# Kernel optimization log

Measured on AMD Instinct MI355X. Metric: run time of the kernel, lower is better.

Reference implementation:

```python
import jax, jax.numpy as jnp
import numpy as np

NUE, NAP, E = 512, 1024, 524288
D, OC, HID, PH = 4, 64, 32, 4  # raw feat dim, out_channels, out//2, power hid


def _lin(key, fi, fo):
    k1, k2 = jax.random.split(key)
    s = 1.0 / np.sqrt(fi)
    W = jax.random.uniform(k1, (fi, fo), minval=-s, maxval=s, dtype=jnp.float32)
    b = jax.random.uniform(k2, (fo,), minval=-s, maxval=s, dtype=jnp.float32)
    return W, b


_LAYER_SPECS = [
    ("c1_msg", D + D, HID), ("c1_upd", HID + D, OC - D), ("c1_ew", 3 * D, OC - D),
    ("c2_msg", OC + D, HID), ("c2_upd", HID + D, OC - D), ("c2_ew", D + OC + D, OC - D),
    ("c3u_msg", 2 * OC, HID), ("c3u_upd", HID + OC, OC - D), ("c3u_ew", 3 * OC, OC - D),
    ("c3d_msg", 2 * OC, HID), ("c3d_upd", HID + OC, OC - D), ("c3d_ew", 3 * OC, OC - D),
    ("pe1", OC, PH), ("pe2", PH, 1),
]


def setup_inputs() -> dict:
    key = jax.random.key(0)
    ks = jax.random.split(key, 24)
    inp = {}
    inp["x_ue"] = jax.random.normal(ks[0], (NUE, D), dtype=jnp.float32)
    inp["x_ap"] = jax.random.normal(ks[1], (NAP, D), dtype=jnp.float32)
    inp["ea_up"] = jax.random.normal(ks[2], (E, D), dtype=jnp.float32)
    inp["ea_down"] = jax.random.normal(ks[3], (E, D), dtype=jnp.float32)
    inp["ei_up_src"] = jax.random.randint(ks[4], (E,), 0, NUE, dtype=jnp.int32)
    inp["ei_up_dst"] = jax.random.randint(ks[5], (E,), 0, NAP, dtype=jnp.int32)
    inp["ei_down_src"] = jax.random.randint(ks[6], (E,), 0, NAP, dtype=jnp.int32)
    inp["ei_down_dst"] = jax.random.randint(ks[7], (E,), 0, NUE, dtype=jnp.int32)
    for i, (n, fi, fo) in enumerate(_LAYER_SPECS):
        W, b = _lin(ks[8 + i], fi, fo)
        inp[n + "_W"] = W
        inp[n + "_b"] = b
    inp["pe_ln_g"] = jnp.ones((PH,), dtype=jnp.float32)
    inp["pe_ln_b"] = jnp.zeros((PH,), dtype=jnp.float32)
    return inp


def _lrelu(x):
    return jnp.where(x >= 0, x, 0.1 * x)


def _mlp1(x, W, b):  # one MLP block: Linear -> LeakyReLU(0.1) (dropout = eval identity)
    return _lrelu(x @ W + b)


def _conv_step(x_src, x_dst, ea, src_idx, dst_idx, n_dst,
               msg_W, msg_b, upd_W, upd_b, ew_W, ew_b, residual):
    xj = x_src[src_idx]                                   # [E, d_src] gather
    m = _mlp1(jnp.concatenate([xj, ea], axis=1), msg_W, msg_b)  # [E, HID]
    agg = jax.ops.segment_sum(m, dst_idx, num_segments=n_dst)   # scatter-add -> [n_dst, HID]
    tmp = _mlp1(jnp.concatenate([x_dst, agg], axis=1), upd_W, upd_b)  # [n_dst, OC-D]
    if residual:
        tmp = tmp + x_dst[:, D:]
    new_x_dst = jnp.concatenate([x_dst[:, :D], tmp], axis=1)     # [n_dst, OC]
    xi = x_dst[dst_idx]                                   # old x_dst per torch code
    e = _mlp1(jnp.concatenate([xj, ea, xi], axis=1), ew_W, ew_b)  # [E, OC-D]
    new_ea = jnp.concatenate([ea[:, :D], e], axis=1)             # [E, OC]
    return new_x_dst, new_ea


def _layernorm(x, g, b, eps=1e-5):
    mu = jnp.mean(x, axis=-1, keepdims=True)
    var = jnp.mean(jnp.square(x - mu), axis=-1, keepdims=True)
    return (x - mu) * jax.lax.rsqrt(var + eps) * g + b


def reference(x_ue, x_ap, ea_up, ea_down,
              ei_up_src, ei_up_dst, ei_down_src, ei_down_dst,
              c1_msg_W, c1_msg_b, c1_upd_W, c1_upd_b, c1_ew_W, c1_ew_b,
              c2_msg_W, c2_msg_b, c2_upd_W, c2_upd_b, c2_ew_W, c2_ew_b,
              c3u_msg_W, c3u_msg_b, c3u_upd_W, c3u_upd_b, c3u_ew_W, c3u_ew_b,
              c3d_msg_W, c3d_msg_b, c3d_upd_W, c3d_upd_b, c3d_ew_W, c3d_ew_b,
              pe1_W, pe1_b, pe2_W, pe2_b, pe_ln_g, pe_ln_b):
    # conv1: UE --up--> AP
    x_ap, ea_up = _conv_step(x_ue, x_ap, ea_up, ei_up_src, ei_up_dst, NAP,
                             c1_msg_W, c1_msg_b, c1_upd_W, c1_upd_b, c1_ew_W, c1_ew_b, False)
    # conv2: AP --down--> UE
    x_ue, ea_down = _conv_step(x_ap, x_ue, ea_down, ei_down_src, ei_down_dst, NUE,
                               c2_msg_W, c2_msg_b, c2_upd_W, c2_upd_b, c2_ew_W, c2_ew_b, False)
    # conv3 handles both edge types (residual since src_dim == out_channels)
    x_ap, ea_up = _conv_step(x_ue, x_ap, ea_up, ei_up_src, ei_up_dst, NAP,
                             c3u_msg_W, c3u_msg_b, c3u_upd_W, c3u_upd_b, c3u_ew_W, c3u_ew_b, True)
    x_ue, ea_down = _conv_step(x_ap, x_ue, ea_down, ei_down_src, ei_down_dst, NUE,
                               c3d_msg_W, c3d_msg_b, c3d_upd_W, c3d_upd_b, c3d_ew_W, c3d_ew_b, True)
    # power head on down edges: Lin -> LayerNorm -> LeakyReLU -> Lin
    h = _lrelu(_layernorm(ea_down @ pe1_W + pe1_b, pe_ln_g, pe_ln_b))
    power = h @ pe2_W + pe2_b                                   # [E, 1]
    ea_down = jnp.concatenate([ea_down[:, :D], power], axis=1)  # [E, D+1]
    return (x_ue, x_ap, ea_up, ea_down)
```

## Files before the change

### kernel.cpp

```cpp
#include <hip/hip_runtime.h>

typedef __attribute__((ext_vector_type(8))) short bf16x8;
typedef __attribute__((ext_vector_type(4))) float f32x4;

static constexpr int EN   = 524288;
static constexpr int NUE_ = 512;
static constexpr int NAP_ = 1024;
static constexpr int HID_ = 32;
static constexpr int OD_  = 60;
static constexpr int OC_  = 64;
static constexpr int NB_  = 256;
static constexpr int CH_  = EN / NB_;

__device__ __forceinline__ unsigned short f2bf(float x) {
  unsigned int u = __float_as_uint(x);
  return (unsigned short)((u + 0x7fffu + ((u >> 16) & 1u)) >> 16);
}
__device__ __forceinline__ float bf2f(unsigned int u) {
  return __uint_as_float(u << 16);
}

__global__ __launch_bounds__(256)
void prep_all(const float* __restrict__ c3u_ew, const float* __restrict__ c3u_msg,
              const float* __restrict__ c3d_ew, const float* __restrict__ c3d_msg,
              unsigned short* __restrict__ we3u, unsigned short* __restrict__ wm3u,
              unsigned short* __restrict__ we3d, unsigned short* __restrict__ wm3d)
{
  const int blk = blockIdx.x, t = threadIdx.x;
  const float* W; unsigned short* out; int NREAL, NPAD, i;
  if (blk < 16)      { W = c3u_ew;  out = we3u; NREAL = 60; NPAD = 64; i = blk * 256 + t; }
  else if (blk < 24) { W = c3u_msg; out = wm3u; NREAL = 32; NPAD = 32; i = (blk - 16) * 256 + t; }
  else if (blk < 40) { W = c3d_ew;  out = we3d; NREAL = 60; NPAD = 64; i = (blk - 24) * 256 + t; }
  else               { W = c3d_msg; out = wm3d; NREAL = 32; NPAD = 32; i = (blk - 40) * 256 + t; }
  if (i >= NPAD * 64) return;
  int n = i >> 6, k = i & 63;
  float v = (n < NREAL) ? W[(size_t)(64 + k) * NREAL + n] : 0.f;
  out[i] = f2bf(v);
}

__global__ __launch_bounds__(256)
void lhist2(const int* __restrict__ up_dst, const int* __restrict__ dn_dst,
            int* __restrict__ bh_up, int* __restrict__ bh_dn,
            unsigned short* __restrict__ lr_up, unsigned short* __restrict__ lr_dn)
{
  __shared__ int h[NAP_];
  const int t = threadIdx.x;
  const bool up = blockIdx.x < NB_;
  const int b = up ? blockIdx.x : blockIdx.x - NB_;
  const int NBINS = up ? NAP_ : NUE_;
  const int* dst = up ? up_dst : dn_dst;
  int* bh = up ? bh_up : bh_dn;
  unsigned short* lrank = up ? lr_up : lr_dn;
  for (int i = t; i < NBINS; i += 256) h[i] = 0;
  __syncthreads();
  const int base = b * CH_;
  #pragma unroll 1
  for (int i = t; i < CH_; i += 256)
    lrank[base + i] = (unsigned short)atomicAdd(&h[dst[base + i]], 1);
  __syncthreads();
  for (int i = t; i < NBINS; i += 256)
    bh[(size_t)i * NB_ + b] = h[i];
}

__global__ __launch_bounds__(64)
void bscanA2(int* __restrict__ bh_up, int* __restrict__ bh_dn,
             int* __restrict__ bs_up, int* __restrict__ bs_dn)
{
  const bool up = blockIdx.x < NAP_;
  const int bin = up ? blockIdx.x : blockIdx.x - NAP_;
  int* bh = up ? bh_up : bh_dn;
  int* binsum = up ? bs_up : bs_dn;
  const int l = threadIdx.x;
  int4 v = *reinterpret_cast<int4*>(&bh[(size_t)bin * NB_ + l * 4]);
  const int s0 = v.x, s1 = s0 + v.y, s2 = s1 + v.z, s3 = s2 + v.w;
  int inc = s3;
  #pragma unroll
  for (int d2 = 1; d2 < 64; d2 <<= 1) {
    int n = __shfl_up(inc, d2, 64);
    if (l >= d2) inc += n;
  }
  const int exc = inc - s3;
  int4 o; o.x = exc; o.y = exc + s0; o.z = exc + s1; o.w = exc + s2;
  *reinterpret_cast<int4*>(&bh[(size_t)bin * NB_ + l * 4]) = o;
  if (l == 63) binsum[bin] = inc;
}

__global__ __launch_bounds__(256)
void bscanB2(const int* __restrict__ bs_up, int* __restrict__ off_up,
             const int* __restrict__ bs_dn, int* __restrict__ off_dn)
{
  const bool up = blockIdx.x == 0;
  const int NBINS = up ? NAP_ : NUE_;
  const int K = NBINS / 256;
  const int* binsum = up ? bs_up : bs_dn;
  int* off = up ? off_up : off_dn;
  __shared__ int wtot[4];
  const int t = threadIdx.x, lane = t & 63, wid = t >> 6;
  int loc[4]; int s = 0;
  for (int k = 0; k < K; ++k) { loc[k] = binsum[t * K + k]; s += loc[k]; }
  int inc = s;
  #pragma unroll
  for (int d2 = 1; d2 < 64; d2 <<= 1) {
    int n = __shfl_up(inc, d2, 64);
    if (lane >= d2) inc += n;
  }
  if (lane == 63) wtot[wid] = inc;
  __syncthreads();
  int woff = 0;
  #pragma unroll
  for (int ww = 0; ww < 4; ++ww) if (ww < wid) woff += wtot[ww];
  int a = woff + inc - s;
  for (int k = 0; k < K; ++k) { off[t * K + k] = a; a += loc[k]; }
  if (t == 255) off[NBINS] = a;
}

__global__ __launch_bounds__(256)
void rankc2(const int* __restrict__ up_dst, const int* __restrict__ up_src,
            const int* __restrict__ dn_dst, const int* __restrict__ dn_src,
            const unsigned short* __restrict__ lr_up, const unsigned short* __restrict__ lr_dn,
            const int* __restrict__ bh_up, const int* __restrict__ bh_dn,
            const int* __restrict__ off_up, const int* __restrict__ off_dn,
            int* __restrict__ rank_dn,
            int* __restrict__ perm_up, int* __restrict__ srcP_up, int* __restrict__ dstP_up,
            int* __restrict__ perm_dn, int* __restrict__ srcP_dn, int* __restrict__ dstP_dn)
{
  const int gid = blockIdx.x * 256 + threadIdx.x;
  const bool up = gid < EN;
  const int e = up ? gid : gid - EN;
  const int* dst = up ? up_dst : dn_dst;
  const int* src = up ? up_src : dn_src;
  const unsigned short* lrank = up ? lr_up : lr_dn;
  const int* bh = up ? bh_up : bh_dn;
  const int* off = up ? off_up : off_dn;
  const int blk = e / CH_;
  const int d = dst[e];
  const int rk = off[d] + bh[(size_t)d * NB_ + blk] + (int)lrank[e];
  if (up) {
    perm_up[rk] = e; srcP_up[rk] = src[e]; dstP_up[rk] = d;
  } else {
    rank_dn[e] = rk;
    perm_dn[rk] = e; srcP_dn[rk] = src[e]; dstP_dn[rk] = d;
  }
}

__global__ __launch_bounds__(256)
void tabs0(const float* __restrict__ x_ue, const float* __restrict__ x_ap,
           const float* __restrict__ c1_ew, const float* __restrict__ c1_msg,
           const float* __restrict__ c1_ew_b, const float* __restrict__ c1_msg_b,
           const float* __restrict__ c2_ew, const float* __restrict__ c2_ew_b,
           float* __restrict__ Y1j, float* __restrict__ Y1i,
           float* __restrict__ Y1m, float* __restrict__ Y2i)
{
  const int tid = blockIdx.x * 256 + threadIdx.x;
  if (tid < NUE_) {
    const float4 x = *reinterpret_cast<const float4*>(x_ue + (size_t)tid * 4);
    const float xv[4] = {x.x, x.y, x.z, x.w};
    for (int o = 0; o < OD_; ++o) {
      float a = 0.f, b = c2_ew_b[o];
      #pragma unroll
      for (int k = 0; k < 4; ++k) {
        a = fmaf(xv[k], c1_ew[k * OD_ + o], a);
        b = fmaf(xv[k], c2_ew[(68 + k) * OD_ + o], b);
      }
      Y1j[(size_t)tid * OD_ + o] = a;
      Y2i[(size_t)tid * OD_ + o] = b;
    }
    for (int o = 0; o < HID_; ++o) {
      float m = c1_msg_b[o];
      #pragma unroll
      for (int k = 0; k < 4; ++k) m = fmaf(xv[k], c1_msg[k * HID_ + o], m);
      Y1m[(size_t)tid * HID_ + o] = m;
    }
  } else if (tid < NUE_ + NAP_) {
    const int r = tid - NUE_;
    const float4 x = *reinterpret_cast<const float4*>(x_ap + (size_t)r * 4);
    const float xv[4] = {x.x, x.y, x.z, x.w};
    for (int o = 0; o < OD_; ++o) {
      float a = c1_ew_b[o];
      #pragma unroll
      for (int k = 0; k < 4; ++k) a = fmaf(xv[k], c1_ew[(8 + k) * OD_ + o], a);
      Y1i[(size_t)r * OD_ + o] = a;
    }
  }
}

__global__ __launch_bounds__(256)
void edge12(const float* __restrict__ ea_in,
            const int* __restrict__ perm, const int* __restrict__ srcP,
            const int* __restrict__ dstP,
            const float* __restrict__ Yje, const float* __restrict__ Yie,
            const float* __restrict__ Ym,
            const float* __restrict__ We,
            const float* __restrict__ Wm,
            unsigned int* __restrict__ msg32,
            unsigned short* __restrict__ outB)
{
  __shared__ unsigned short Eb[64 * 72];
  const int t = threadIdx.x;
  const int sBase = blockIdx.x * 64;
  const int r = t >> 2, j = t & 3;
  const int slot = sBase + r;
  const int e = perm[slot];
  const int s = srcP[slot], d = dstP[slot];
  const float4 ea = *reinterpret_cast<const float4*>(ea_in + (size_t)e * 4);
  const float eav[4] = {ea.x, ea.y, ea.z, ea.w};

  const int c0 = j * 15;
  float acc[15];
  #pragma unroll
  for (int c = 0; c < 15; ++c)
    acc[c] = Yje[(size_t)s * OD_ + c0 + c] + Yie[(size_t)d * OD_ + c0 + c];
  #pragma unroll
  for (int k = 0; k < 4; ++k)
    #pragma unroll
    for (int c = 0; c < 15; ++c)
      acc[c] = fmaf(eav[k], We[k * OD_ + c0 + c], acc[c]);
  #pragma unroll
  for (int c = 0; c < 15; ++c) {
    float v = acc[c] >= 0.f ? acc[c] : 0.1f * acc[c];
    Eb[r * 72 + 4 + c0 + c] = f2bf(v);
  }
  if (j == 0) {
    Eb[r * 72 + 0] = f2bf(ea.x); Eb[r * 72 + 1] = f2bf(ea.y);
    Eb[r * 72 + 2] = f2bf(ea.z); Eb[r * 72 + 3] = f2bf(ea.w);
  }
  const int m0 = j * 8;
  float m[8];
  #pragma unroll
  for (int c = 0; c < 8; ++c) m[c] = Ym[(size_t)s * HID_ + m0 + c];
  #pragma unroll
  for (int k = 0; k < 4; ++k)
    #pragma unroll
    for (int c = 0; c < 8; ++c)
      m[c] = fmaf(eav[k], Wm[k * HID_ + m0 + c], m[c]);
  #pragma unroll
  for (int c = 0; c < 8; ++c) m[c] = m[c] >= 0.f ? m[c] : 0.1f * m[c];
  uint4 mv;
  mv.x = ((unsigned)f2bf(m[1]) << 16) | f2bf(m[0]);
  mv.y = ((unsigned)f2bf(m[3]) << 16) | f2bf(m[2]);
  mv.z = ((unsigned)f2bf(m[5]) << 16) | f2bf(m[4]);
  mv.w = ((unsigned)f2bf(m[7]) << 16) | f2bf(m[6]);
  *reinterpret_cast<uint4*>(msg32 + (size_t)slot * 16 + j * 4) = mv;
  __syncthreads();

  #pragma unroll
  for (int i = 0; i < 2; ++i) {
    int idx = t + i * 256;
    int row = idx >> 3, ch = idx & 7;
    *reinterpret_cast<uint4*>(outB + (size_t)(sBase + row) * OC_ + ch * 8) =
        *reinterpret_cast<const uint4*>(&Eb[row * 72 + ch * 8]);
  }
}

template<bool FUSE>
__global__ __launch_bounds__(256)
void edge3(const unsigned short* __restrict__ eaB,
           const float* __restrict__ ea0_src,
           const int* __restrict__ perm,
           const int* __restrict__ srcP, const int* __restrict__ dstP,
           const unsigned short* __restrict__ Wet, const unsigned short* __restrict__ Wmt,
           const float* __restrict__ Yje, const float* __restrict__ Yie,
           const float* __restrict__ Ym,
           unsigned int* __restrict__ msg32,
           float* __restrict__ ea_out,
           float* __restrict__ pT,
           const float* __restrict__ pe1_W)
{
  const int t = threadIdx.x, l = t & 63, w = t >> 6;
  const int lr = l & 15, lkb = l >> 4;
  const int sW = blockIdx.x * 256 + w * 64;

  bf16x8 be[4][2], bm[2][2];
  #pragma unroll
  for (int nt = 0; nt < 4; ++nt)
    #pragma unroll
    for (int kk = 0; kk < 2; ++kk)
      be[nt][kk] = *reinterpret_cast<const bf16x8*>(Wet + (nt * 16 + lr) * 64 + kk * 32 + lkb * 8);
  #pragma unroll
  for (int nt = 0; nt < 2; ++nt)
    #pragma unroll
    for (int kk = 0; kk < 2; ++kk)
      bm[nt][kk] = *reinterpret_cast<const bf16x8*>(Wmt + (nt * 16 + lr) * 64 + kk * 32 + lkb * 8);

  #pragma unroll 1
  for (int tile = 0; tile < 4; ++tile) {
    const int s0t = sW + tile * 16;
    const unsigned short* ar = eaB + (size_t)(s0t + lr) * OC_ + lkb * 8;
    bf16x8 a[2];
    a[0] = *reinterpret_cast<const bf16x8*>(ar);
    a[1] = *reinterpret_cast<const bf16x8*>(ar + 32);

    f32x4 accE[4] = {f32x4{0,0,0,0}, f32x4{0,0,0,0}, f32x4{0,0,0,0}, f32x4{0,0,0,0}};
    f32x4 accM[2] = {f32x4{0,0,0,0}, f32x4{0,0,0,0}};
    #pragma unroll
    for (int kk = 0; kk < 2; ++kk) {
      #pragma unroll
      for (int nt = 0; nt < 4; ++nt)
        accE[nt] = __builtin_amdgcn_mfma_f32_16x16x32_bf16(a[kk], be[nt][kk], accE[nt], 0, 0, 0);
      #pragma unroll
      for (int nt = 0; nt < 2; ++nt)
        accM[nt] = __builtin_amdgcn_mfma_f32_16x16x32_bf16(a[kk], bm[nt][kk], accM[nt], 0, 0, 0);
    }
    #pragma unroll
    for (int r = 0; r < 4; ++r) {
      const int sl = s0t + lkb * 4 + r;
      const int s = srcP[sl], d = dstP[sl];
      float v0 = accM[0][r] + Ym[(size_t)s * HID_ + lr];
      float v1 = accM[1][r] + Ym[(size_t)s * HID_ + 16 + lr];
      v0 = v0 >= 0.f ? v0 : 0.1f * v0;
      v1 = v1 >= 0.f ? v1 : 0.1f * v1;
      const int q0 = (2 * lr) & 15, q1 = (2 * lr + 1) & 15;
      float t00 = __shfl(v0, q0, 16), t10 = __shfl(v1, q0, 16);
      float t01 = __shfl(v0, q1, 16), t11 = __shfl(v1, q1, 16);
      float lo = (lr < 8) ? t00 : t10;
      float hi = (lr < 8) ? t01 : t11;
      msg32[(size_t)sl * 16 + lr] = ((unsigned)f2bf(hi) << 16) | f2bf(lo);

      float val[4];
      #pragma unroll
      for (int nt = 0; nt < 4; ++nt) {
        int col = nt * 16 + lr;
        float v = (col < OD_)
            ? accE[nt][r] + Yje[(size_t)s * OD_ + col] + Yie[(size_t)d * OD_ + col]
            : 0.f;
        val[nt] = v >= 0.f ? v : 0.1f * v;
      }
      if constexpr (!FUSE) {
        const int e = perm[sl];
        #pragma unroll
        for (int nt = 0; nt < 4; ++nt) {
          int col = nt * 16 + lr;
          if (col < OD_) ea_out[(size_t)e * OC_ + 4 + col] = val[nt];
        }
        if (lr == 0) {
          float4 ea0 = *reinterpret_cast<const float4*>(ea0_src + (size_t)e * 4);
          *reinterpret_cast<float4*>(ea_out + (size_t)e * OC_) = ea0;
        }
      } else {
        float p4[4] = {0.f, 0.f, 0.f, 0.f};
        #pragma unroll
        for (int nt = 0; nt < 4; ++nt) {
          int col = nt * 16 + lr;
          if (col < OD_) {
            #pragma unroll
            for (int jj = 0; jj < 4; ++jj)
              p4[jj] = fmaf(val[nt], pe1_W[(4 + col) * 4 + jj], p4[jj]);
          }
        }
        #pragma unroll
        for (int mk = 1; mk < 16; mk <<= 1) {
          #pragma unroll
          for (int jj = 0; jj < 4; ++jj)
            p4[jj] += __shfl_xor(p4[jj], mk, 64);
        }
        if (lr == 0)
          *reinterpret_cast<float4*>(pT + (size_t)sl * 4) =
              make_float4(p4[0], p4[1], p4[2], p4[3]);
      }
    }
  }
}

template<int LX, bool RES>
__device__ __forceinline__
void nodeup_body(int d, int t,
                 const float* __restrict__ x_in,
                 const unsigned int* __restrict__ msg32,
                 const int* __restrict__ off,
                 const float* __restrict__ W, const float* __restrict__ b,
                 float* __restrict__ x_out,
                 const float* WtA, float* YA,
                 const float* WtB, const float* bB, float* YB,
                 const float* WtC, const float* bC, float* YC)
{
  __shared__ float Pb[16][32];
  __shared__ float Ag[32];
  __shared__ float Xr[LX];
  __shared__ float Xn[OC_];
  const int beg = off[d], end = off[d + 1];
  const int c = t & 15, g = t >> 4;
  float px = 0.f, py = 0.f;
  for (int i = beg + g; i < end; i += 16) {
    unsigned u = msg32[(size_t)i * 16 + c];
    px += bf2f(u & 0xffffu);
    py += bf2f(u >> 16);
  }
  Pb[g][2 * c] = px; Pb[g][2 * c + 1] = py;
  if (t < LX) Xr[t] = x_in[(size_t)d * LX + t];
  __syncthreads();
  if (t < 32) {
    float s = 0.f;
    #pragma unroll
    for (int g2 = 0; g2 < 16; ++g2) s += Pb[g2][t];
    Ag[t] = s;
  }
  __syncthreads();
  if (t < OD_) {
    float acc = b[t];
    #pragma unroll 4
    for (int k = 0; k < LX; ++k) acc = fmaf(Xr[k], W[k * OD_ + t], acc);
    #pragma unroll 4
    for (int k = 0; k < HID_; ++k) acc = fmaf(Ag[k], W[(LX + k) * OD_ + t], acc);
    acc = acc >= 0.f ? acc : 0.1f * acc;
    if constexpr (RES) acc += Xr[4 + t];
    x_out[(size_t)d * OC_ + 4 + t] = acc;
    Xn[4 + t] = acc;
  } else if (t < OC_) {
    x_out[(size_t)d * OC_ + (t - OD_)] = Xr[t - OD_];
    Xn[t - OD_] = Xr[t - OD_];
  }
  if (WtA == nullptr) return;
  __syncthreads();
  if (t < OD_) {
    float a = 0.f;
    #pragma unroll 4
    for (int k = 0; k < OC_; ++k) a = fmaf(Xn[k], WtA[k * OD_ + t], a);
    YA[(size_t)d * OD_ + t] = a;
  } else if (t >= 64 && t < 96) {
    const int cc = t - 64;
    float a = bB[cc];
    #pragma unroll 4
    for (int k = 0; k < OC_; ++k) a = fmaf(Xn[k], WtB[k * HID_ + cc], a);
    YB[(size_t)d * HID_ + cc] = a;
  } else if (WtC != nullptr && t >= 128 && t < 188) {
    const int cc = t - 128;
    float a = bC[cc];
    #pragma unroll 4
    for (int k = 0; k < OC_; ++k) a = fmaf(Xn[k], WtC[k * OD_ + cc], a);
    YC[(size_t)d * OD_ + cc] = a;
  }
}

template<int LX, bool RES>
__global__ __launch_bounds__(256)
void nodeupT(const float* __restrict__ x_in, const unsigned int* __restrict__ msg32,
             const int* __restrict__ off,
             const float* __restrict__ W, const float* __restrict__ b,
             float* __restrict__ x_out,
             const float* WtA, float* YA,
             const float* WtB, const float* bB, float* YB,
             const float* WtC, const float* bC, float* YC)
{
  nodeup_body<LX, RES>(blockIdx.x, threadIdx.x, x_in, msg32, off, W, b, x_out,
                       WtA, YA, WtB, bB, YB, WtC, bC, YC);
}

__global__ __launch_bounds__(256)
void nodeup_pow(const float* __restrict__ x_in, const unsigned int* __restrict__ msg32,
                const int* __restrict__ off,
                const float* __restrict__ W, const float* __restrict__ b,
                float* __restrict__ x_out,
                const float* __restrict__ ea0_src, const int* __restrict__ rank,
                const float* __restrict__ pT,
                const float* __restrict__ pe1_W, const float* __restrict__ pe1_b,
                const float* __restrict__ pe2_W, const float* __restrict__ pe2_b,
                const float* __restrict__ ln_g, const float* __restrict__ ln_b,
                float* __restrict__ outp)
{
  if (blockIdx.x < NUE_) {
    nodeup_body<OC_, true>(blockIdx.x, threadIdx.x, x_in, msg32, off, W, b, x_out,
                           nullptr, nullptr, nullptr, nullptr, nullptr,
                           nullptr, nullptr, nullptr);
    return;
  }
  const int e = (blockIdx.x - NUE_) * 256 + threadIdx.x;
  const int rk = rank[e];
  const float4 p4 = *reinterpret_cast<const float4*>(pT + (size_t)rk * 4);
  const float4 ea0 = *reinterpret_cast<const float4*>(ea0_src + (size_t)e * 4);
  const float pv[4] = {p4.x, p4.y, p4.z, p4.w};
  float v4[4];
  #pragma unroll
  for (int jj = 0; jj < 4; ++jj)
    v4[jj] = pv[jj] + pe1_b[jj]
           + ea0.x * pe1_W[0 * 4 + jj] + ea0.y * pe1_W[1 * 4 + jj]
           + ea0.z * pe1_W[2 * 4 + jj] + ea0.w * pe1_W[3 * 4 + jj];
  const float mu = 0.25f * (v4[0] + v4[1] + v4[2] + v4[3]);
  float var = 0.f;
  #pragma unroll
  for (int jj = 0; jj < 4; ++jj) { float dd = v4[jj] - mu; var = fmaf(dd, dd, var); }
  var *= 0.25f;
  const float rstd = rsqrtf(var + 1e-5f);
  float p = pe2_b[0];
  #pragma unroll
  for (int jj = 0; jj < 4; ++jj) {
    float h = (v4[jj] - mu) * rstd * ln_g[jj] + ln_b[jj];
    h = h >= 0.f ? h : 0.1f * h;
    p = fmaf(h, pe2_W[jj], p);
  }
  float* orow = outp + (size_t)e * 5;
  orow[0] = ea0.x; orow[1] = ea0.y; orow[2] = ea0.z; orow[3] = ea0.w;
  orow[4] = p;
}

extern "C" void kernel_launch(void* const* d_in, const int* in_sizes, int n_in,
                              void* d_out, int out_size, void* d_ws, size_t ws_size,
                              hipStream_t stream)
{
  const float* x_ue    = (const float*)d_in[0];
  const float* x_ap    = (const float*)d_in[1];
  const float* ea_up   = (const float*)d_in[2];
  const float* ea_down = (const float*)d_in[3];
  const int* up_src = (const int*)d_in[4];
  const int* up_dst = (const int*)d_in[5];
  const int* dn_src = (const int*)d_in[6];
  const int* dn_dst = (const int*)d_in[7];
  const float* c1_msg_W = (const float*)d_in[8];  const float* c1_msg_b = (const float*)d_in[9];
  const float* c1_upd_W = (const float*)d_in[10]; const float* c1_upd_b = (const float*)d_in[11];
  const float* c1_ew_W  = (const float*)d_in[12]; const float* c1_ew_b  = (const float*)d_in[13];
  const float* c2_msg_W = (const float*)d_in[14]; const float* c2_msg_b = (const float*)d_in[15];
  const float* c2_upd_W = (const float*)d_in[16]; const float* c2_upd_b = (const float*)d_in[17];
  const float* c2_ew_W  = (const float*)d_in[18]; const float* c2_ew_b  = (const float*)d_in[19];
  const float* c3u_msg_W= (const float*)d_in[20]; const float* c3u_msg_b= (const float*)d_in[21];
  const float* c3u_upd_W= (const float*)d_in[22]; const float* c3u_upd_b= (const float*)d_in[23];
  const float* c3u_ew_W = (const float*)d_in[24]; const float* c3u_ew_b = (const float*)d_in[25];
  const float* c3d_msg_W= (const float*)d_in[26]; const float* c3d_msg_b= (const float*)d_in[27];
  const float* c3d_upd_W= (const float*)d_in[28]; const float* c3d_upd_b= (const float*)d_in[29];
  const float* c3d_ew_W = (const float*)d_in[30]; const float* c3d_ew_b = (const float*)d_in[31];
  const float* pe1_W = (const float*)d_in[32]; const float* pe1_b = (const float*)d_in[33];
  const float* pe2_W = (const float*)d_in[34]; const float* pe2_b = (const float*)d_in[35];
  const float* ln_g  = (const float*)d_in[36]; const float* ln_b  = (const float*)d_in[37];

  float* out    = (float*)d_out;
  float* x_ue_o = out;
  float* x_ap_o = out + (size_t)NUE_ * OC_;
  float* ea_up_o = x_ap_o + (size_t)NAP_ * OC_;
  float* ea_dn_o = ea_up_o + (size_t)EN * OC_;

  int* ip = (int*)d_ws;
  int* rank_dn = ip; ip += EN;
  int* perm_up = ip; ip += EN;
  int* src_upP = ip; ip += EN;
  int* dst_upP = ip; ip += EN;
  int* perm_dn = ip; ip += EN;
  int* src_dnP = ip; ip += EN;
  int* dst_dnP = ip; ip += EN;
  int* bh_up   = ip; ip += NAP_ * NB_;
  int* bh_dn   = ip; ip += NUE_ * NB_;
  int* off_up  = ip; ip += NAP_ + 1;
  int* off_dn  = ip; ip += NUE_ + 1;
  int* bs_up   = ip; ip += NAP_;
  int* bs_dn   = ip; ip += NUE_;
  unsigned short* lr_up = (unsigned short*)ip; ip += EN / 2;
  unsigned short* lr_dn = (unsigned short*)ip; ip += EN / 2;
  float* p = (float*)ip;
  float* Y1j = p;  p += NUE_ * OD_;  float* Y1i = p; p += NAP_ * OD_;  float* Y1m = p; p += NUE_ * HID_;
  float* Y2j = p;  p += NAP_ * OD_;  float* Y2i = p; p += NUE_ * OD_;  float* Y2m = p; p += NAP_ * HID_;
  float* Y3uj = p; p += NUE_ * OD_;  float* Y3ui = p; p += NAP_ * OD_; float* Y3um = p; p += NUE_ * HID_;
  float* Y3dj = p; p += NAP_ * OD_;  float* Y3di = p; p += NUE_ * OD_; float* Y3dm = p; p += NAP_ * HID_;
  float* pT = p;   p += (size_t)EN * 4;
  unsigned short* us = (unsigned short*)p;
  unsigned short* ea_up_bf = us;  us += (size_t)EN * OC_;
  unsigned short* ea_dn_bf = us;  us += (size_t)EN * OC_;
  unsigned short* we3u = us; us += 64 * 64;
  unsigned short* wm3u = us; us += 32 * 64;
  unsigned short* we3d = us; us += 64 * 64;
  unsigned short* wm3d = us; us += 32 * 64;
  unsigned int* msg32 = (unsigned int*)(((size_t)us + 15) & ~(size_t)15);

  const dim3 blk(256);
  const dim3 eg12(EN / 64);
  const dim3 ege(EN / 256);

  lhist2<<<dim3(2 * NB_), blk, 0, stream>>>(up_dst, dn_dst, bh_up, bh_dn, lr_up, lr_dn);
  bscanA2<<<dim3(NAP_ + NUE_), dim3(64), 0, stream>>>(bh_up, bh_dn, bs_up, bs_dn);
  bscanB2<<<dim3(2), blk, 0, stream>>>(bs_up, off_up, bs_dn, off_dn);
  rankc2<<<dim3(2 * EN / 256), blk, 0, stream>>>(
      up_dst, up_src, dn_dst, dn_src, lr_up, lr_dn, bh_up, bh_dn, off_up, off_dn,
      rank_dn, perm_up, src_upP, dst_upP, perm_dn, src_dnP, dst_dnP);

  prep_all<<<dim3(48), blk, 0, stream>>>(c3u_ew_W, c3u_msg_W, c3d_ew_W, c3d_msg_W,
                                         we3u, wm3u, we3d, wm3d);
  tabs0<<<dim3(8), blk, 0, stream>>>(x_ue, x_ap, c1_ew_W, c1_msg_W, c1_ew_b, c1_msg_b,
                                     c2_ew_W, c2_ew_b, Y1j, Y1i, Y1m, Y2i);

  edge12<<<eg12, blk, 0, stream>>>(
      ea_up, perm_up, src_upP, dst_upP, Y1j, Y1i, Y1m,
      c1_ew_W + 4 * OD_, c1_msg_W + 4 * HID_, msg32, ea_up_bf);
  nodeupT<4, false><<<dim3(NAP_), blk, 0, stream>>>(
      x_ap, msg32, off_up, c1_upd_W, c1_upd_b, x_ap_o,
      c2_ew_W, Y2j, c2_msg_W, c2_msg_b, Y2m,
      c3u_ew_W + 128 * OD_, c3u_ew_b, Y3ui);

  edge12<<<eg12, blk, 0, stream>>>(
      ea_down, perm_dn, src_dnP, dst_dnP, Y2j, Y2i, Y2m,
      c2_ew_W + 64 * OD_, c2_msg_W + 64 * HID_, msg32, ea_dn_bf);
  nodeupT<4, false><<<dim3(NUE_), blk, 0, stream>>>(
      x_ue, msg32, off_dn, c2_upd_W, c2_upd_b, x_ue_o,
      c3u_ew_W, Y3uj, c3u_msg_W, c3u_msg_b, Y3um,
      c3d_ew_W + 128 * OD_, c3d_ew_b, Y3di);

  edge3<false><<<ege, blk, 0, stream>>>(
      ea_up_bf, ea_up, perm_up, src_upP, dst_upP, we3u, wm3u,
      Y3uj, Y3ui, Y3um, msg32, ea_up_o, nullptr, nullptr);
  nodeupT<64, true><<<dim3(NAP_), blk, 0, stream>>>(
      x_ap_o, msg32, off_up, c3u_upd_W, c3u_upd_b, x_ap_o,
      c3d_ew_W, Y3dj, c3d_msg_W, c3d_msg_b, Y3dm,
      nullptr, nullptr, nullptr);

  edge3<true><<<ege, blk, 0, stream>>>(
      ea_dn_bf, nullptr, nullptr, src_dnP, dst_dnP, we3d, wm3d,
      Y3dj, Y3di, Y3dm, msg32, nullptr, pT, pe1_W);
  nodeup_pow<<<dim3(NUE_ + EN / 256), blk, 0, stream>>>(
      x_ue_o, msg32, off_dn, c3d_upd_W, c3d_upd_b, x_ue_o,
      ea_down, rank_dn, pT, pe1_W, pe1_b, pe2_W, pe2_b, ln_g, ln_b, ea_dn_o);
}
```

Before: 471.5 us.

## Fuse conv1/conv2 edge pass with per-destination aggregation and node update

Replaces the edge12 plus nodeupT pair for conv1 and conv2 with a single e12n kernel that runs one block per destination node. Each block walks that node's sorted edge segment, writes the edge features, and accumulates messages in registers, which removes the msg32 round trip and one launch per conv. The small prep and table kernels are folded into extra blocks of the histogram kernel, and edge3 now prefetches its A tiles and src/dst indices ahead of the MFMA loop. The trade-off is parallelism: conv1 gets only 1024 blocks and conv2 only 512, each with a serial loop over about 512 or 1024 edges, so load balance and occupancy may suffer compared with the edge-parallel grid.

```diff
diff --git a/kernel.cpp b/kernel.cpp
--- a/kernel.cpp
+++ b/kernel.cpp
@@ -21,30 +21,69 @@
 }
 
 __global__ __launch_bounds__(256)
-void prep_all(const float* __restrict__ c3u_ew, const float* __restrict__ c3u_msg,
-              const float* __restrict__ c3d_ew, const float* __restrict__ c3d_msg,
-              unsigned short* __restrict__ we3u, unsigned short* __restrict__ wm3u,
-              unsigned short* __restrict__ we3d, unsigned short* __restrict__ wm3d)
-{
-  const int blk = blockIdx.x, t = threadIdx.x;
-  const float* W; unsigned short* out; int NREAL, NPAD, i;
-  if (blk < 16)      { W = c3u_ew;  out = we3u; NREAL = 60; NPAD = 64; i = blk * 256 + t; }
-  else if (blk < 24) { W = c3u_msg; out = wm3u; NREAL = 32; NPAD = 32; i = (blk - 16) * 256 + t; }
-  else if (blk < 40) { W = c3d_ew;  out = we3d; NREAL = 60; NPAD = 64; i = (blk - 24) * 256 + t; }
-  else               { W = c3d_msg; out = wm3d; NREAL = 32; NPAD = 32; i = (blk - 40) * 256 + t; }
-  if (i >= NPAD * 64) return;
-  int n = i >> 6, k = i & 63;
-  float v = (n < NREAL) ? W[(size_t)(64 + k) * NREAL + n] : 0.f;
-  out[i] = f2bf(v);
-}
-
-__global__ __launch_bounds__(256)
-void lhist2(const int* __restrict__ up_dst, const int* __restrict__ dn_dst,
-            int* __restrict__ bh_up, int* __restrict__ bh_dn,
-            unsigned short* __restrict__ lr_up, unsigned short* __restrict__ lr_dn)
+void lhist2x(const int* __restrict__ up_dst, const int* __restrict__ dn_dst,
+             int* __restrict__ bh_up, int* __restrict__ bh_dn,
+             unsigned short* __restrict__ lr_up, unsigned short* __restrict__ lr_dn,
+             const float* __restrict__ c3u_ew, const float* __restrict__ c3u_msg,
+             const float* __restrict__ c3d_ew, const float* __restrict__ c3d_msg,
+             unsigned short* __restrict__ we3u, unsigned short* __restrict__ wm3u,
+             unsigned short* __restrict__ we3d, unsigned short* __restrict__ wm3d,
+             const float* __restrict__ x_ue, const float* __restrict__ x_ap,
+             const float* __restrict__ c1_ew, const float* __restrict__ c1_msg,
+             const float* __restrict__ c1_ew_b, const float* __restrict__ c1_msg_b,
+             const float* __restrict__ c2_ew, const float* __restrict__ c2_ew_b,
+             float* __restrict__ Y1j, float* __restrict__ Y1i,
+             float* __restrict__ Y1m, float* __restrict__ Y2i)
 {
   __shared__ int h[NAP_];
   const int t = threadIdx.x;
+  if (blockIdx.x >= 2 * NB_) {
+    const int xb = blockIdx.x - 2 * NB_;
+    if (xb < 48) {
+      const float* W; unsigned short* out; int NREAL, NPAD, i;
+      if (xb < 16)      { W = c3u_ew;  out = we3u; NREAL = 60; NPAD = 64; i = xb * 256 + t; }
+      else if (xb < 24) { W = c3u_msg; out = wm3u; NREAL = 32; NPAD = 32; i = (xb - 16) * 256 + t; }
+      else if (xb < 40) { W = c3d_ew;  out = we3d; NREAL = 60; NPAD = 64; i = (xb - 24) * 256 + t; }
+      else              { W = c3d_msg; out = wm3d; NREAL = 32; NPAD = 32; i = (xb - 40) * 256 + t; }
+      if (i >= NPAD * 64) return;
+      int n = i >> 6, k = i & 63;
+      float v = (n < NREAL) ? W[(size_t)(64 + k) * NREAL + n] : 0.f;
+      out[i] = f2bf(v);
+    } else {
+      const int tid = (xb - 48) * 256 + t;
+      if (tid < NUE_) {
+        const float4 x = *reinterpret_cast<const float4*>(x_ue + (size_t)tid * 4);
+        const float xv[4] = {x.x, x.y, x.z, x.w};
+        for (int o = 0; o < OD_; ++o) {
+          float a = 0.f, bb = c2_ew_b[o];
+          #pragma unroll
+          for (int k = 0; k < 4; ++k) {
+            a = fmaf(xv[k], c1_ew[k * OD_ + o], a);
+            bb = fmaf(xv[k], c2_ew[(68 + k) * OD_ + o], bb);
+          }
+          Y1j[(size_t)tid * OD_ + o] = a;
+          Y2i[(size_t)tid * OD_ + o] = bb;
+        }
+        for (int o = 0; o < HID_; ++o) {
+          float m = c1_msg_b[o];
+          #pragma unroll
+          for (int k = 0; k < 4; ++k) m = fmaf(xv[k], c1_msg[k * HID_ + o], m);
+          Y1m[(size_t)tid * HID_ + o] = m;
+        }
+      } else if (tid < NUE_ + NAP_) {
+        const int r = tid - NUE_;
+        const float4 x = *reinterpret_cast<const float4*>(x_ap + (size_t)r * 4);
+        const float xv[4] = {x.x, x.y, x.z, x.w};
+        for (int o = 0; o < OD_; ++o) {
+          float a = c1_ew_b[o];
+          #pragma unroll
+          for (int k = 0; k < 4; ++k) a = fmaf(xv[k], c1_ew[(8 + k) * OD_ + o], a);
+          Y1i[(size_t)r * OD_ + o] = a;
+        }
+      }
+    }
+    return;
+  }
   const bool up = blockIdx.x < NB_;
   const int b = up ? blockIdx.x : blockIdx.x - NB_;
   const int NBINS = up ? NAP_ : NUE_;
@@ -144,111 +183,135 @@
 }
 
 __global__ __launch_bounds__(256)
-void tabs0(const float* __restrict__ x_ue, const float* __restrict__ x_ap,
-           const float* __restrict__ c1_ew, const float* __restrict__ c1_msg,
-           const float* __restrict__ c1_ew_b, const float* __restrict__ c1_msg_b,
-           const float* __restrict__ c2_ew, const float* __restrict__ c2_ew_b,
-           float* __restrict__ Y1j, float* __restrict__ Y1i,
-           float* __restrict__ Y1m, float* __restrict__ Y2i)
-{
-  const int tid = blockIdx.x * 256 + threadIdx.x;
-  if (tid < NUE_) {
-    const float4 x = *reinterpret_cast<const float4*>(x_ue + (size_t)tid * 4);
-    const float xv[4] = {x.x, x.y, x.z, x.w};
-    for (int o = 0; o < OD_; ++o) {
-      float a = 0.f, b = c2_ew_b[o];
+void e12n(const float* __restrict__ ea_in,
+          const int* __restrict__ perm, const int* __restrict__ srcP,
+          const int* __restrict__ off,
+          const float* __restrict__ Yje, const float* __restrict__ Yie,
+          const float* __restrict__ Ym,
+          const float* __restrict__ We,
+          const float* __restrict__ Wm,
+          unsigned short* __restrict__ outB,
+          const float* __restrict__ x_in,
+          const float* __restrict__ W, const float* __restrict__ b,
+          float* __restrict__ x_out,
+          const float* __restrict__ WtA, float* __restrict__ YA,
+          const float* __restrict__ WtB, const float* __restrict__ bB, float* __restrict__ YB,
+          const float* __restrict__ WtC, const float* __restrict__ bC, float* __restrict__ YC)
+{
+  __shared__ unsigned short Eb[64 * 72];
+  __shared__ float RedF[64][33];
+  __shared__ float Part[8][33];
+  __shared__ float Ag[32];
+  __shared__ float Xr[4];
+  __shared__ float Xn[OC_];
+  const int d = blockIdx.x, t = threadIdx.x;
+  const int beg = off[d], end = off[d + 1];
+  const int r = t >> 2, j = t & 3;
+  const int c0 = j * 15, m0 = j * 8;
+  if (t < 4) Xr[t] = x_in[(size_t)d * 4 + t];
+  float yie[15];
+  #pragma unroll
+  for (int c = 0; c < 15; ++c) yie[c] = Yie[(size_t)d * OD_ + c0 + c];
+  float am[8] = {0.f, 0.f, 0.f, 0.f, 0.f, 0.f, 0.f, 0.f};
+
+  for (int sb = beg; sb < end; sb += 64) {
+    const int slot = sb + r;
+    const bool act = slot < end;
+    const int e = act ? perm[slot] : 0;
+    const int s = act ? srcP[slot] : 0;
+    float4 ea = act ? *reinterpret_cast<const float4*>(ea_in + (size_t)e * 4)
+                    : make_float4(0.f, 0.f, 0.f, 0.f);
+    const float eav[4] = {ea.x, ea.y, ea.z, ea.w};
+    float acc[15];
+    #pragma unroll
+    for (int c = 0; c < 15; ++c) acc[c] = Yje[(size_t)s * OD_ + c0 + c] + yie[c];
+    #pragma unroll
+    for (int k = 0; k < 4; ++k)
       #pragma unroll
-      for (int k = 0; k < 4; ++k) {
-        a = fmaf(xv[k], c1_ew[k * OD_ + o], a);
-        b = fmaf(xv[k], c2_ew[(68 + k) * OD_ + o], b);
+      for (int c = 0; c < 15; ++c)
+        acc[c] = fmaf(eav[k], We[k * OD_ + c0 + c], acc[c]);
+    if (act) {
+      #pragma unroll
+      for (int c = 0; c < 15; ++c) {
+        float v = acc[c] >= 0.f ? acc[c] : 0.1f * acc[c];
+        Eb[r * 72 + 4 + c0 + c] = f2bf(v);
       }
-      Y1j[(size_t)tid * OD_ + o] = a;
-      Y2i[(size_t)tid * OD_ + o] = b;
+      if (j == 0) {
+        Eb[r * 72 + 0] = f2bf(ea.x); Eb[r * 72 + 1] = f2bf(ea.y);
+        Eb[r * 72 + 2] = f2bf(ea.z); Eb[r * 72 + 3] = f2bf(ea.w);
+      }
     }
-    for (int o = 0; o < HID_; ++o) {
-      float m = c1_msg_b[o];
+    float m[8];
+    #pragma unroll
+    for (int c = 0; c < 8; ++c) m[c] = Ym[(size_t)s * HID_ + m0 + c];
+    #pragma unroll
+    for (int k = 0; k < 4; ++k)
       #pragma unroll
-      for (int k = 0; k < 4; ++k) m = fmaf(xv[k], c1_msg[k * HID_ + o], m);
-      Y1m[(size_t)tid * HID_ + o] = m;
+      for (int c = 0; c < 8; ++c)
+        m[c] = fmaf(eav[k], Wm[k * HID_ + m0 + c], m[c]);
+    if (act) {
+      #pragma unroll
+      for (int c = 0; c < 8; ++c)
+        am[c] += m[c] >= 0.f ? m[c] : 0.1f * m[c];
     }
-  } else if (tid < NUE_ + NAP_) {
-    const int r = tid - NUE_;
-    const float4 x = *reinterpret_cast<const float4*>(x_ap + (size_t)r * 4);
-    const float xv[4] = {x.x, x.y, x.z, x.w};
-    for (int o = 0; o < OD_; ++o) {
-      float a = c1_ew_b[o];
-      #pragma unroll
-      for (int k = 0; k < 4; ++k) a = fmaf(xv[k], c1_ew[(8 + k) * OD_ + o], a);
-      Y1i[(size_t)r * OD_ + o] = a;
+    __syncthreads();
+    const int nact = end - sb < 64 ? end - sb : 64;
+    for (int idx = t; idx < nact * 8; idx += 256) {
+      int row = idx >> 3, ch = idx & 7;
+      *reinterpret_cast<uint4*>(outB + (size_t)(sb + row) * OC_ + ch * 8) =
+          *reinterpret_cast<const uint4*>(&Eb[row * 72 + ch * 8]);
     }
-  }
-}
-
-__global__ __launch_bounds__(256)
-void edge12(const float* __restrict__ ea_in,
-            const int* __restrict__ perm, const int* __restrict__ srcP,
-            const int* __restrict__ dstP,
-            const float* __restrict__ Yje, const float* __restrict__ Yie,
-            const float* __restrict__ Ym,
-            const float* __restrict__ We,
-            const float* __restrict__ Wm,
-            unsigned int* __restrict__ msg32,
-            unsigned short* __restrict__ outB)
-{
-  __shared__ unsigned short Eb[64 * 72];
-  const int t = threadIdx.x;
-  const int sBase = blockIdx.x * 64;
-  const int r = t >> 2, j = t & 3;
-  const int slot = sBase + r;
-  const int e = perm[slot];
-  const int s = srcP[slot], d = dstP[slot];
-  const float4 ea = *reinterpret_cast<const float4*>(ea_in + (size_t)e * 4);
-  const float eav[4] = {ea.x, ea.y, ea.z, ea.w};
-
-  const int c0 = j * 15;
-  float acc[15];
-  #pragma unroll
-  for (int c = 0; c < 15; ++c)
-    acc[c] = Yje[(size_t)s * OD_ + c0 + c] + Yie[(size_t)d * OD_ + c0 + c];
-  #pragma unroll
-  for (int k = 0; k < 4; ++k)
-    #pragma unroll
-    for (int c = 0; c < 15; ++c)
-      acc[c] = fmaf(eav[k], We[k * OD_ + c0 + c], acc[c]);
-  #pragma unroll
-  for (int c = 0; c < 15; ++c) {
-    float v = acc[c] >= 0.f ? acc[c] : 0.1f * acc[c];
-    Eb[r * 72 + 4 + c0 + c] = f2bf(v);
-  }
-  if (j == 0) {
-    Eb[r * 72 + 0] = f2bf(ea.x); Eb[r * 72 + 1] = f2bf(ea.y);
-    Eb[r * 72 + 2] = f2bf(ea.z); Eb[r * 72 + 3] = f2bf(ea.w);
-  }
-  const int m0 = j * 8;
-  float m[8];
-  #pragma unroll
-  for (int c = 0; c < 8; ++c) m[c] = Ym[(size_t)s * HID_ + m0 + c];
-  #pragma unroll
-  for (int k = 0; k < 4; ++k)
-    #pragma unroll
-    for (int c = 0; c < 8; ++c)
-      m[c] = fmaf(eav[k], Wm[k * HID_ + m0 + c], m[c]);
-  #pragma unroll
-  for (int c = 0; c < 8; ++c) m[c] = m[c] >= 0.f ? m[c] : 0.1f * m[c];
-  uint4 mv;
-  mv.x = ((unsigned)f2bf(m[1]) << 16) | f2bf(m[0]);
-  mv.y = ((unsigned)f2bf(m[3]) << 16) | f2bf(m[2]);
-  mv.z = ((unsigned)f2bf(m[5]) << 16) | f2bf(m[4]);
-  mv.w = ((unsigned)f2bf(m[7]) << 16) | f2bf(m[6]);
-  *reinterpret_cast<uint4*>(msg32 + (size_t)slot * 16 + j * 4) = mv;
-  __syncthreads();
-
-  #pragma unroll
-  for (int i = 0; i < 2; ++i) {
-    int idx = t + i * 256;
-    int row = idx >> 3, ch = idx & 7;
-    *reinterpret_cast<uint4*>(outB + (size_t)(sBase + row) * OC_ + ch * 8) =
-        *reinterpret_cast<const uint4*>(&Eb[row * 72 + ch * 8]);
+    __syncthreads();
+  }
+  #pragma unroll
+  for (int c = 0; c < 8; ++c) RedF[r][m0 + c] = am[c];
+  __syncthreads();
+  {
+    const int col = t & 31, g = t >> 5;
+    float s = 0.f;
+    #pragma unroll
+    for (int r2 = 0; r2 < 8; ++r2) s += RedF[g * 8 + r2][col];
+    Part[g][col] = s;
+  }
+  __syncthreads();
+  if (t < 32) {
+    float s = 0.f;
+    #pragma unroll
+    for (int g2 = 0; g2 < 8; ++g2) s += Part[g2][t];
+    Ag[t] = s;
+  }
+  __syncthreads();
+  if (t < OD_) {
+    float acc = b[t];
+    #pragma unroll
+    for (int k = 0; k < 4; ++k) acc = fmaf(Xr[k], W[k * OD_ + t], acc);
+    #pragma unroll 4
+    for (int k = 0; k < HID_; ++k) acc = fmaf(Ag[k], W[(4 + k) * OD_ + t], acc);
+    acc = acc >= 0.f ? acc : 0.1f * acc;
+    x_out[(size_t)d * OC_ + 4 + t] = acc;
+    Xn[4 + t] = acc;
+  } else if (t < OC_) {
+    x_out[(size_t)d * OC_ + (t - OD_)] = Xr[t - OD_];
+    Xn[t - OD_] = Xr[t - OD_];
+  }
+  __syncthreads();
+  if (t < OD_) {
+    float a = 0.f;
+    #pragma unroll 4
+    for (int k = 0; k < OC_; ++k) a = fmaf(Xn[k], WtA[k * OD_ + t], a);
+    YA[(size_t)d * OD_ + t] = a;
+  } else if (t >= 64 && t < 96) {
+    const int cc = t - 64;
+    float a = bB[cc];
+    #pragma unroll 4
+    for (int k = 0; k < OC_; ++k) a = fmaf(Xn[k], WtB[k * HID_ + cc], a);
+    YB[(size_t)d * HID_ + cc] = a;
+  } else if (t >= 128 && t < 188) {
+    const int cc = t - 128;
+    float a = bC[cc];
+    #pragma unroll 4
+    for (int k = 0; k < OC_; ++k) a = fmaf(Xn[k], WtC[k * OD_ + cc], a);
+    YC[(size_t)d * OD_ + cc] = a;
   }
 }
 
@@ -270,6 +333,13 @@
   const int lr = l & 15, lkb = l >> 4;
   const int sW = blockIdx.x * 256 + w * 64;
 
+  bf16x8 a[4][2];
+  #pragma unroll
+  for (int tile = 0; tile < 4; ++tile) {
+    const unsigned short* ar = eaB + (size_t)(sW + tile * 16 + lr) * OC_ + lkb * 8;
+    a[tile][0] = *reinterpret_cast<const bf16x8*>(ar);
+    a[tile][1] = *reinterpret_cast<const bf16x8*>(ar + 32);
+  }
   bf16x8 be[4][2], bm[2][2];
   #pragma unroll
   for (int nt = 0; nt < 4; ++nt)
@@ -285,26 +355,27 @@
   #pragma unroll 1
   for (int tile = 0; tile < 4; ++tile) {
     const int s0t = sW + tile * 16;
-    const unsigned short* ar = eaB + (size_t)(s0t + lr) * OC_ + lkb * 8;
-    bf16x8 a[2];
-    a[0] = *reinterpret_cast<const bf16x8*>(ar);
-    a[1] = *reinterpret_cast<const bf16x8*>(ar + 32);
-
+    int sA[4], dA[4];
+    #pragma unroll
+    for (int r = 0; r < 4; ++r) {
+      sA[r] = srcP[s0t + lkb * 4 + r];
+      dA[r] = dstP[s0t + lkb * 4 + r];
+    }
     f32x4 accE[4] = {f32x4{0,0,0,0}, f32x4{0,0,0,0}, f32x4{0,0,0,0}, f32x4{0,0,0,0}};
     f32x4 accM[2] = {f32x4{0,0,0,0}, f32x4{0,0,0,0}};
     #pragma unroll
     for (int kk = 0; kk < 2; ++kk) {
       #pragma unroll
       for (int nt = 0; nt < 4; ++nt)
-        accE[nt] = __builtin_amdgcn_mfma_f32_16x16x32_bf16(a[kk], be[nt][kk], accE[nt], 0, 0, 0);
+        accE[nt] = __builtin_amdgcn_mfma_f32_16x16x32_bf16(a[tile][kk], be[nt][kk], accE[nt], 0, 0, 0);
       #pragma unroll
       for (int nt = 0; nt < 2; ++nt)
-        accM[nt] = __builtin_amdgcn_mfma_f32_16x16x32_bf16(a[kk], bm[nt][kk], accM[nt], 0, 0, 0);
+        accM[nt] = __builtin_amdgcn_mfma_f32_16x16x32_bf16(a[tile][kk], bm[nt][kk], accM[nt], 0, 0, 0);
     }
     #pragma unroll
     for (int r = 0; r < 4; ++r) {
       const int sl = s0t + lkb * 4 + r;
-      const int s = srcP[sl], d = dstP[sl];
+      const int s = sA[r], d = dA[r];
       float v0 = accM[0][r] + Ym[(size_t)s * HID_ + lr];
       float v1 = accM[1][r] + Ym[(size_t)s * HID_ + 16 + lr];
       v0 = v0 >= 0.f ? v0 : 0.1f * v0;
@@ -370,8 +441,7 @@
                  const float* __restrict__ W, const float* __restrict__ b,
                  float* __restrict__ x_out,
                  const float* WtA, float* YA,
-                 const float* WtB, const float* bB, float* YB,
-                 const float* WtC, const float* bC, float* YC)
+                 const float* WtB, const float* bB, float* YB)
 {
   __shared__ float Pb[16][32];
   __shared__ float Ag[32];
@@ -422,12 +492,6 @@
     #pragma unroll 4
     for (int k = 0; k < OC_; ++k) a = fmaf(Xn[k], WtB[k * HID_ + cc], a);
     YB[(size_t)d * HID_ + cc] = a;
-  } else if (WtC != nullptr && t >= 128 && t < 188) {
-    const int cc = t - 128;
-    float a = bC[cc];
-    #pragma unroll 4
-    for (int k = 0; k < OC_; ++k) a = fmaf(Xn[k], WtC[k * OD_ + cc], a);
-    YC[(size_t)d * OD_ + cc] = a;
   }
 }
 
@@ -438,11 +502,10 @@
              const float* __restrict__ W, const float* __restrict__ b,
              float* __restrict__ x_out,
              const float* WtA, float* YA,
-             const float* WtB, const float* bB, float* YB,
-             const float* WtC, const float* bC, float* YC)
+             const float* WtB, const float* bB, float* YB)
 {
   nodeup_body<LX, RES>(blockIdx.x, threadIdx.x, x_in, msg32, off, W, b, x_out,
-                       WtA, YA, WtB, bB, YB, WtC, bC, YC);
+                       WtA, YA, WtB, bB, YB);
 }
 
 __global__ __launch_bounds__(256)
@@ -459,8 +522,7 @@
 {
   if (blockIdx.x < NUE_) {
     nodeup_body<OC_, true>(blockIdx.x, threadIdx.x, x_in, msg32, off, W, b, x_out,
-                           nullptr, nullptr, nullptr, nullptr, nullptr,
-                           nullptr, nullptr, nullptr);
+                           nullptr, nullptr, nullptr, nullptr, nullptr);
     return;
   }
   const int e = (blockIdx.x - NUE_) * 256 + threadIdx.x;
@@ -558,34 +620,30 @@
   unsigned int* msg32 = (unsigned int*)(((size_t)us + 15) & ~(size_t)15);
 
   const dim3 blk(256);
-  const dim3 eg12(EN / 64);
   const dim3 ege(EN / 256);
 
-  lhist2<<<dim3(2 * NB_), blk, 0, stream>>>(up_dst, dn_dst, bh_up, bh_dn, lr_up, lr_dn);
+  lhist2x<<<dim3(2 * NB_ + 56), blk, 0, stream>>>(
+      up_dst, dn_dst, bh_up, bh_dn, lr_up, lr_dn,
+      c3u_ew_W, c3u_msg_W, c3d_ew_W, c3d_msg_W, we3u, wm3u, we3d, wm3d,
+      x_ue, x_ap, c1_ew_W, c1_msg_W, c1_ew_b, c1_msg_b, c2_ew_W, c2_ew_b,
+      Y1j, Y1i, Y1m, Y2i);
   bscanA2<<<dim3(NAP_ + NUE_), dim3(64), 0, stream>>>(bh_up, bh_dn, bs_up, bs_dn);
   bscanB2<<<dim3(2), blk, 0, stream>>>(bs_up, off_up, bs_dn, off_dn);
   rankc2<<<dim3(2 * EN / 256), blk, 0, stream>>>(
       up_dst, up_src, dn_dst, dn_src, lr_up, lr_dn, bh_up, bh_dn, off_up, off_dn,
       rank_dn, perm_up, src_upP, dst_upP, perm_dn, src_dnP, dst_dnP);
 
-  prep_all<<<dim3(48), blk, 0, stream>>>(c3u_ew_W, c3u_msg_W, c3d_ew_W, c3d_msg_W,
-                                         we3u, wm3u, we3d, wm3d);
-  tabs0<<<dim3(8), blk, 0, stream>>>(x_ue, x_ap, c1_ew_W, c1_msg_W, c1_ew_b, c1_msg_b,
-                                     c2_ew_W, c2_ew_b, Y1j, Y1i, Y1m, Y2i);
-
-  edge12<<<eg12, blk, 0, stream>>>(
-      ea_up, perm_up, src_upP, dst_upP, Y1j, Y1i, Y1m,
-      c1_ew_W + 4 * OD_, c1_msg_W + 4 * HID_, msg32, ea_up_bf);
-  nodeupT<4, false><<<dim3(NAP_), blk, 0, stream>>>(
-      x_ap, msg32, off_up, c1_upd_W, c1_upd_b, x_ap_o,
+  e12n<<<dim3(NAP_), blk, 0, stream>>>(
+      ea_up, perm_up, src_upP, off_up, Y1j, Y1i, Y1m,
+      c1_ew_W + 4 * OD_, c1_msg_W + 4 * HID_, ea_up_bf,
+      x_ap, c1_upd_W, c1_upd_b, x_ap_o,
       c2_ew_W, Y2j, c2_msg_W, c2_msg_b, Y2m,
       c3u_ew_W + 128 * OD_, c3u_ew_b, Y3ui);
 
-  edge12<<<eg12, blk, 0, stream>>>(
-      ea_down, perm_dn, src_dnP, dst_dnP, Y2j, Y2i, Y2m,
-      c2_ew_W + 64 * OD_, c2_msg_W + 64 * HID_, msg32, ea_dn_bf);
-  nodeupT<4, false><<<dim3(NUE_), blk, 0, stream>>>(
-      x_ue, msg32, off_dn, c2_upd_W, c2_upd_b, x_ue_o,
+  e12n<<<dim3(NUE_), blk, 0, stream>>>(
+      ea_down, perm_dn, src_dnP, off_dn, Y2j, Y2i, Y2m,
+      c2_ew_W + 64 * OD_, c2_msg_W + 64 * HID_, ea_dn_bf,
+      x_ue, c2_upd_W, c2_upd_b, x_ue_o,
       c3u_ew_W, Y3uj, c3u_msg_W, c3u_msg_b, Y3um,
       c3d_ew_W + 128 * OD_, c3d_ew_b, Y3di);
 
@@ -594,8 +652,7 @@
       Y3uj, Y3ui, Y3um, msg32, ea_up_o, nullptr, nullptr);
   nodeupT<64, true><<<dim3(NAP_), blk, 0, stream>>>(
       x_ap_o, msg32, off_up, c3u_upd_W, c3u_upd_b, x_ap_o,
-      c3d_ew_W, Y3dj, c3d_msg_W, c3d_msg_b, Y3dm,
-      nullptr, nullptr, nullptr);
+      c3d_ew_W, Y3dj, c3d_msg_W, c3d_msg_b, Y3dm);
 
   edge3<true><<<ege, blk, 0, stream>>>(
       ea_dn_bf, nullptr, nullptr, src_dnP, dst_dnP, we3d, wm3d,
```

New measurement: 597.4 us. 26.7% more time.
